# Kernel optimization log

Measured on AMD Instinct MI355X. Metric: run time of the kernel, lower is better.

The kernel has to match this reference:

```python
import jax, jax.numpy as jnp
import numpy as np

T, N, F0, H0, H1 = 8, 50000, 128, 128, 64
NNZ, E = 800000, 1000000


def setup_inputs() -> dict:
    key = jax.random.key(0)
    ks = jax.random.split(key, 24)
    s = 0.05  # param scale so sigmoid/tanh gates are not fully saturated
    inp = {
        "X": jax.random.normal(ks[0], (T, N, F0), jnp.float32),
        "A_rows": jax.random.randint(ks[1], (T, NNZ), 0, N, jnp.int32),
        "A_cols": jax.random.randint(ks[2], (T, NNZ), 0, N, jnp.int32),
        "A_val": jax.random.uniform(ks[3], (T, NNZ), jnp.float32),
        "edge_time": jax.random.randint(ks[4], (E,), 0, T, jnp.int32),
        "edge_src": jax.random.randint(ks[5], (E,), 0, N, jnp.int32),
        "edge_trg": jax.random.randint(ks[6], (E,), 0, N, jnp.int32),
        "p": jax.random.normal(ks[7], (F0,), jnp.float32),
        "W_Z": s * jax.random.normal(ks[8], (F0, F0), jnp.float32),
        "U_Z": s * jax.random.normal(ks[9], (F0, F0), jnp.float32),
        "B_Z": s * jax.random.normal(ks[10], (F0, H0), jnp.float32),
        "W_R": s * jax.random.normal(ks[11], (F0, F0), jnp.float32),
        "U_R": s * jax.random.normal(ks[12], (F0, F0), jnp.float32),
        "B_R": s * jax.random.normal(ks[13], (F0, H0), jnp.float32),
        "W_H": s * jax.random.normal(ks[14], (F0, F0), jnp.float32),
        "U_H": s * jax.random.normal(ks[15], (F0, F0), jnp.float32),
        "B_H": s * jax.random.normal(ks[16], (F0, H0), jnp.float32),
        "W_init": s * jax.random.normal(ks[17], (F0, H0), jnp.float32),
        "U": s * jax.random.normal(ks[18], (2 * H0, H1), jnp.float32),
    }
    return inp


def reference(X, A_rows, A_cols, A_val, edge_time, edge_src, edge_trg,
              p, W_Z, U_Z, B_Z, W_R, U_R, B_R, W_H, U_H, B_H, W_init, U):
    Tn, Nn, _ = X.shape
    k = W_init.shape[1]  # topk size == columns of evolving weight
    p_hat = p / jnp.linalg.norm(p)

    def step(W, inputs):
        Xs, rows, cols, vals = inputs  # Xs: [N,F0]; rows/cols/vals: [NNZ]
        # summarize: top-k node rows weighted by projection score
        y = Xs @ p_hat                       # [N]
        topv, idx = jax.lax.top_k(y, k)
        Z = (Xs[idx] * topv[:, None]).T      # [F0,k]
        # GRU-style weight evolution on the [F0,k] weight matrix
        Zg = jax.nn.sigmoid(W_Z @ Z + U_Z @ W + B_Z)
        R = jax.nn.sigmoid(W_R @ Z + U_R @ W + B_R)
        Ht = jnp.tanh(W_H @ Z + U_H @ (R * W) + B_H)
        W_new = (1.0 - Zg) * W + Zg * Ht
        # sparse GCN conv: (A @ Xs) @ W_new  via gather + segment_sum
        AH = jax.ops.segment_sum(vals[:, None] * Xs[cols], rows,
                                 num_segments=Nn)  # [N,F0]
        return W_new, AH @ W_new                   # Y_t: [N,H0]

    W_fin, Y = jax.lax.scan(step, W_init, (X, A_rows, A_cols, A_val))
    Yf = Y.reshape(Tn * Nn, -1)                    # [T*N,H0]
    flat_src = edge_time * Nn + edge_src
    flat_trg = edge_time * Nn + edge_trg
    Y_mat = jnp.concatenate([Yf[flat_src], Yf[flat_trg]], axis=1)  # [E,2*H0]
    output = Y_mat @ U                              # [E,H1]
    return output, W_fin
```

## Files before the change

### kernel.cpp

```cpp
#include <hip/hip_runtime.h>
#include <math.h>

#define T_ 8
#define N_ 50000
#define F0_ 128
#define H0_ 128
#define H1_ 64
#define NNZ_ 800000
#define E_ 1000000
#define K_ 128
#define CAP_ 3072
#define NB 391
#define BCH 8192

__device__ inline unsigned ford(float f) {
    unsigned b = __float_as_uint(f);
    return (b & 0x80000000u) ? ~b : (b | 0x80000000u);
}
__device__ inline float funord(unsigned u) {
    unsigned b = (u & 0x80000000u) ? (u & 0x7fffffffu) : ~u;
    return __uint_as_float(b);
}
__device__ inline unsigned bfr(float f) {
    unsigned u = __float_as_uint(f);
    return (u + 0x7fffu + ((u >> 16) & 1u)) >> 16;
}
__device__ inline unsigned bfpack(float lo, float hi) { return bfr(lo) | (bfr(hi) << 16); }
__device__ inline float bflo(unsigned u) { return __uint_as_float(u << 16); }
__device__ inline float bfhi(unsigned u) { return __uint_as_float(u & 0xffff0000u); }

__global__ void k_phat(const float* p, float* p_hat) {
    __shared__ float s[128];
    int i = threadIdx.x;
    float v = p[i];
    s[i] = v * v;
    __syncthreads();
    for (int off = 64; off > 0; off >>= 1) {
        if (i < off) s[i] += s[i + off];
        __syncthreads();
    }
    p_hat[i] = v / sqrtf(s[0]);
}

__global__ void k_y(const float* __restrict__ X, const float* __restrict__ p_hat,
                    float* __restrict__ y, unsigned* __restrict__ Xh) {
    int gid = blockIdx.x * 256 + threadIdx.x;
    int wave = gid >> 6, lane = gid & 63;
    if (wave >= T_ * N_) return;
    const float2* xr = (const float2*)(X + (size_t)wave * F0_);
    float2 a = xr[lane];
    if (Xh) Xh[(size_t)wave * 64 + lane] = bfpack(a.x, a.y);
    float2 ph = ((const float2*)p_hat)[lane];
    float acc = a.x * ph.x + a.y * ph.y;
#pragma unroll
    for (int off = 32; off > 0; off >>= 1) acc += __shfl_down(acc, off);
    if (lane == 0) y[wave] = acc;
}

__global__ __launch_bounds__(1024) void k_topk(const float* __restrict__ y,
                                               float* __restrict__ topv,
                                               int* __restrict__ topidx) {
    int t = blockIdx.x;
    const float* yt = y + (size_t)t * N_;
    __shared__ int hist[256];
    __shared__ int sb1, sAbove, sP, scand;
    __shared__ unsigned cu[CAP_];
    __shared__ int cidx[CAP_];
    int tid = threadIdx.x;

    if (tid < 256) hist[tid] = 0;
    __syncthreads();
    for (int i = tid; i < N_; i += 1024) {
        unsigned u = ford(yt[i]);
        atomicAdd(&hist[u >> 24], 1);
    }
    __syncthreads();
    if (tid == 0) {
        int acc = 0, b = 255;
        for (; b >= 0; b--) { acc += hist[b]; if (acc >= K_) break; }
        sb1 = b;
        sAbove = acc - hist[b];
    }
    __syncthreads();
    int b1 = sb1;
    if (tid < 256) hist[tid] = 0;
    __syncthreads();
    for (int i = tid; i < N_; i += 1024) {
        unsigned u = ford(yt[i]);
        if ((int)(u >> 24) == b1) atomicAdd(&hist[(u >> 16) & 255], 1);
    }
    __syncthreads();
    if (tid == 0) {
        int acc = sAbove, b = 255;
        for (; b >= 0; b--) { acc += hist[b]; if (acc >= K_) break; }
        sP = (b1 << 8) | b;
        scand = 0;
    }
    __syncthreads();
    unsigned P = (unsigned)sP;
    for (int i = tid; i < N_; i += 1024) {
        unsigned u = ford(yt[i]);
        if ((u >> 16) >= P) {
            int pos = atomicAdd(&scand, 1);
            if (pos < CAP_) { cu[pos] = u; cidx[pos] = i; }
        }
    }
    __syncthreads();
    int C = min(scand, CAP_);
    for (int c = tid; c < C; c += 1024) {
        unsigned uc = cu[c];
        int ic = cidx[c];
        int rank = 0;
        for (int o = 0; o < C; o++) {
            unsigned uo = cu[o];
            rank += (uo > uc) || (uo == uc && cidx[o] < ic);
        }
        if (rank < K_) {
            topv[t * K_ + rank] = funord(uc);
            topidx[t * K_ + rank] = ic;
        }
    }
}

__global__ void k_z(const float* __restrict__ X, const float* __restrict__ topv,
                    const int* __restrict__ topidx, float* __restrict__ Z) {
    int gid = blockIdx.x * 256 + threadIdx.x;
    if (gid >= T_ * F0_ * K_) return;
    int j = gid & 127;
    int f = (gid >> 7) & 127;
    int t = gid >> 14;
    int idx = topidx[t * K_ + j];
    float v = topv[t * K_ + j];
    Z[gid] = X[((size_t)(t * N_ + idx)) * F0_ + f] * v;
}

__global__ void k_az(const float* __restrict__ WZ, const float* __restrict__ WR,
                     const float* __restrict__ WH, const float* __restrict__ BZ,
                     const float* __restrict__ BR, const float* __restrict__ BH,
                     const float* __restrict__ Z, float* __restrict__ AZ,
                     float* __restrict__ AR, float* __restrict__ AHo) {
    int gid = blockIdx.x * 256 + threadIdx.x;
    int j = gid & 127;
    int i = (gid >> 7) & 127;
    int t = (gid >> 14) & 7;
    int g = gid >> 17;
    const float* W = (g == 0) ? WZ : (g == 1) ? WR : WH;
    const float* B = (g == 0) ? BZ : (g == 1) ? BR : BH;
    float* Ao = (g == 0) ? AZ : (g == 1) ? AR : AHo;
    const float* Zt = Z + (size_t)t * 16384;
    float acc = B[i * 128 + j];
    for (int k = 0; k < 128; k++) acc += W[i * 128 + k] * Zt[k * 128 + j];
    Ao[(size_t)(t * 128 + i) * 128 + j] = acc;
}

__global__ __launch_bounds__(512) void k_cnt(const int* __restrict__ A_rows,
                                             int* __restrict__ bcnt) {
    __shared__ int cnt[NB];
    int t = blockIdx.y, ci = blockIdx.x;
    int tid = threadIdx.x;
    for (int i = tid; i < NB; i += 512) cnt[i] = 0;
    __syncthreads();
    int e0 = ci * BCH;
#pragma unroll
    for (int k = 0; k < 16; k++) {
        int idx = e0 + tid + k * 512;
        if (idx < NNZ_) atomicAdd(&cnt[A_rows[(size_t)t * NNZ_ + idx] >> 7], 1);
    }
    __syncthreads();
    for (int b = tid; b < NB; b += 512)
        if (cnt[b]) atomicAdd(&bcnt[t * NB + b], cnt[b]);
}

__global__ __launch_bounds__(512) void k_bscan(const int* __restrict__ bcnt,
                                               int* __restrict__ bbase) {
    int t = blockIdx.x;
    int tid = threadIdx.x;
    __shared__ int buf[512];
    int v = (tid < NB) ? bcnt[t * NB + tid] : 0;
    buf[tid] = v;
    __syncthreads();
    for (int off = 1; off < 512; off <<= 1) {
        int x = (tid >= off) ? buf[tid - off] : 0;
        __syncthreads();
        buf[tid] += x;
        __syncthreads();
    }
    if (tid < NB) bbase[t * NB + tid] = buf[tid] - v;
}

__global__ __launch_bounds__(512) void k_binA(const int* __restrict__ A_rows,
                                              const int* __restrict__ A_cols,
                                              const float* __restrict__ A_val,
                                              const int* __restrict__ bbase,
                                              int* __restrict__ bfill,
                                              int2* __restrict__ ebuck) {
    __shared__ int cnt[NB];
    __shared__ int gbase[NB];
    __shared__ int rbase[NB];
    int t = blockIdx.y, ci = blockIdx.x;
    int tid = threadIdx.x;
    for (int i = tid; i < NB; i += 512) cnt[i] = 0;
    __syncthreads();
    unsigned meta[16];
    float val[16];
    int lrank[16];
    int e0 = ci * BCH;
#pragma unroll
    for (int k = 0; k < 16; k++) {
        int idx = e0 + tid + k * 512;
        meta[k] = 0xFFFFFFFFu;
        val[k] = 0.f;
        lrank[k] = 0;
        if (idx < NNZ_) {
            int r = A_rows[(size_t)t * NNZ_ + idx];
            int c = A_cols[(size_t)t * NNZ_ + idx];
            val[k] = A_val[(size_t)t * NNZ_ + idx];
            int b = r >> 7, rlo = r & 127;
            meta[k] = (unsigned)c | ((unsigned)rlo << 16) | ((unsigned)b << 23);
            lrank[k] = atomicAdd(&cnt[b], 1);
        }
    }
    __syncthreads();
    for (int b = tid; b < NB; b += 512) {
        int n = cnt[b];
        gbase[b] = n ? atomicAdd(&bfill[t * NB + b], n) : 0;
        rbase[b] = bbase[t * NB + b];
    }
    __syncthreads();
#pragma unroll
    for (int k = 0; k < 16; k++) {
        if (meta[k] != 0xFFFFFFFFu) {
            int b = meta[k] >> 23;
            ebuck[(size_t)t * NNZ_ + rbase[b] + gbase[b] + lrank[k]] =
                make_int2((int)meta[k], __float_as_int(val[k]));
        }
    }
}

__global__ __launch_bounds__(256) void k_bsort(const int* __restrict__ bbase,
                                               const int* __restrict__ bcnt,
                                               const int2* __restrict__ ebuck,
                                               int2* __restrict__ ecv,
                                               int* __restrict__ row_ptr) {
    __shared__ int rcnt[128];
    __shared__ int rex[128];
    __shared__ int rfill[128];
    __shared__ int sbuf[128];
    int t = blockIdx.y, b = blockIdx.x;
    int tid = threadIdx.x;
    int r0 = b << 7;
    int nrows = min(128, N_ - r0);
    int base = bbase[t * NB + b];
    int n = bcnt[t * NB + b];
    if (tid < 128) {
        rcnt[tid] = 0;
        rfill[tid] = 0;
    }
    __syncthreads();
    const int2* src = ebuck + (size_t)t * NNZ_ + base;
    int2* dst = ecv + (size_t)t * NNZ_ + base;
    for (int i = tid; i < n; i += 256) atomicAdd(&rcnt[(src[i].x >> 16) & 127], 1);
    __syncthreads();
    if (tid < 128) sbuf[tid] = rcnt[tid];
    __syncthreads();
    for (int off = 1; off < 128; off <<= 1) {
        int x = (tid >= off && tid < 128) ? sbuf[tid - off] : 0;
        __syncthreads();
        if (tid < 128) sbuf[tid] += x;
        __syncthreads();
    }
    if (tid < 128) rex[tid] = sbuf[tid] - rcnt[tid];
    if (tid < nrows) row_ptr[(size_t)t * (N_ + 1) + r0 + tid] = base + sbuf[tid] - rcnt[tid];
    if (b == 0 && tid == 0) row_ptr[(size_t)t * (N_ + 1) + N_] = NNZ_;
    __syncthreads();
    for (int i = tid; i < n; i += 256) {
        int2 e = src[i];
        int rlo = (e.x >> 16) & 127;
        int col = e.x & 0xFFFF;
        int pos = rex[rlo] + atomicAdd(&rfill[rlo], 1);
        dst[pos] = make_int2(col, e.y);
    }
}

__global__ __launch_bounds__(256) void k_xwu(const unsigned* __restrict__ Xh,
                                             const float* __restrict__ WU,
                                             unsigned* __restrict__ XWU) {
    __shared__ float AT[32][36];
    __shared__ float WUc[32][128];
    int t = blockIdx.y;
    int rbase = blockIdx.x * 32;
    int tid = threadIdx.x;
    const float* wu = WU + (size_t)t * 16384;
    const unsigned* Xt = Xh + (size_t)t * N_ * 64;
    unsigned* XWUt = XWU + (size_t)t * N_ * 64;
    int cg = tid & 31;
    int rg = tid >> 5;
    float4 acc0 = {0.f, 0.f, 0.f, 0.f};
    float4 acc1 = {0.f, 0.f, 0.f, 0.f};
    float4 acc2 = {0.f, 0.f, 0.f, 0.f};
    float4 acc3 = {0.f, 0.f, 0.f, 0.f};
    int srow = tid >> 3;
    int sk4 = (tid & 7) * 4;
    for (int kc = 0; kc < 128; kc += 32) {
        {
            uint2 u = {0u, 0u};
            int r = rbase + srow;
            if (r < N_) u = *(const uint2*)(Xt + (size_t)r * 64 + (kc >> 1) + (sk4 >> 1));
            AT[sk4 + 0][srow] = bflo(u.x);
            AT[sk4 + 1][srow] = bfhi(u.x);
            AT[sk4 + 2][srow] = bflo(u.y);
            AT[sk4 + 3][srow] = bfhi(u.y);
        }
        {
            const float4* src = (const float4*)(wu + (size_t)kc * 128);
            float4* dst = (float4*)&WUc[0][0];
            dst[tid] = src[tid];
            dst[tid + 256] = src[tid + 256];
            dst[tid + 512] = src[tid + 512];
            dst[tid + 768] = src[tid + 768];
        }
        __syncthreads();
#pragma unroll 4
        for (int kk = 0; kk < 32; kk++) {
            float4 a = *(const float4*)&AT[kk][rg * 4];
            float4 w = *(const float4*)&WUc[kk][cg * 4];
            acc0.x += a.x * w.x; acc0.y += a.x * w.y; acc0.z += a.x * w.z; acc0.w += a.x * w.w;
            acc1.x += a.y * w.x; acc1.y += a.y * w.y; acc1.z += a.y * w.z; acc1.w += a.y * w.w;
            acc2.x += a.z * w.x; acc2.y += a.z * w.y; acc2.z += a.z * w.z; acc2.w += a.z * w.w;
            acc3.x += a.w * w.x; acc3.y += a.w * w.y; acc3.z += a.w * w.z; acc3.w += a.w * w.w;
        }
        __syncthreads();
    }
    int r0 = rbase + rg * 4;
    if (r0 + 0 < N_) {
        uint2 o = {bfpack(acc0.x, acc0.y), bfpack(acc0.z, acc0.w)};
        *(uint2*)(XWUt + (size_t)(r0 + 0) * 64 + cg * 2) = o;
    }
    if (r0 + 1 < N_) {
        uint2 o = {bfpack(acc1.x, acc1.y), bfpack(acc1.z, acc1.w)};
        *(uint2*)(XWUt + (size_t)(r0 + 1) * 64 + cg * 2) = o;
    }
    if (r0 + 2 < N_) {
        uint2 o = {bfpack(acc2.x, acc2.y), bfpack(acc2.z, acc2.w)};
        *(uint2*)(XWUt + (size_t)(r0 + 2) * 64 + cg * 2) = o;
    }
    if (r0 + 3 < N_) {
        uint2 o = {bfpack(acc3.x, acc3.y), bfpack(acc3.z, acc3.w)};
        *(uint2*)(XWUt + (size_t)(r0 + 3) * 64 + cg * 2) = o;
    }
}

__global__ void k_spmm2(const unsigned* __restrict__ XWU, const int* __restrict__ row_ptr,
                        const int2* __restrict__ ecv, unsigned* __restrict__ PQh) {
    int gid = blockIdx.x * 256 + threadIdx.x;
    int wave = gid >> 6, lane = gid & 63;
    if (wave >= T_ * N_) return;
    int t = wave / N_;
    int r = wave - t * N_;
    int s = row_ptr[(size_t)t * (N_ + 1) + r];
    int len = row_ptr[(size_t)t * (N_ + 1) + r + 1] - s;
    const unsigned* Xt = XWU + (size_t)t * N_ * 64 + lane;
    const int2* ev = ecv + (size_t)t * NNZ_;
    float2 acc = {0.f, 0.f};
    for (int base = 0; base < len; base += 64) {
        int nn = min(64, len - base);
        int2 my = {0, 0};
        if (base + lane < len) my = ev[s + base + lane];
        int q = 0;
        for (; q + 16 <= nn; q += 16) {
            int c0 = __shfl(my.x, q + 0);  float v0 = __int_as_float(__shfl(my.y, q + 0));
            int c1 = __shfl(my.x, q + 1);  float v1 = __int_as_float(__shfl(my.y, q + 1));
            int c2 = __shfl(my.x, q + 2);  float v2 = __int_as_float(__shfl(my.y, q + 2));
            int c3 = __shfl(my.x, q + 3);  float v3 = __int_as_float(__shfl(my.y, q + 3));
            int c4 = __shfl(my.x, q + 4);  float v4 = __int_as_float(__shfl(my.y, q + 4));
            int c5 = __shfl(my.x, q + 5);  float v5 = __int_as_float(__shfl(my.y, q + 5));
            int c6 = __shfl(my.x, q + 6);  float v6 = __int_as_float(__shfl(my.y, q + 6));
            int c7 = __shfl(my.x, q + 7);  float v7 = __int_as_float(__shfl(my.y, q + 7));
            int c8 = __shfl(my.x, q + 8);  float v8 = __int_as_float(__shfl(my.y, q + 8));
            int c9 = __shfl(my.x, q + 9);  float v9 = __int_as_float(__shfl(my.y, q + 9));
            int cA = __shfl(my.x, q + 10); float vA = __int_as_float(__shfl(my.y, q + 10));
            int cB = __shfl(my.x, q + 11); float vB = __int_as_float(__shfl(my.y, q + 11));
            int cC = __shfl(my.x, q + 12); float vC = __int_as_float(__shfl(my.y, q + 12));
            int cD = __shfl(my.x, q + 13); float vD = __int_as_float(__shfl(my.y, q + 13));
            int cE = __shfl(my.x, q + 14); float vE = __int_as_float(__shfl(my.y, q + 14));
            int cF = __shfl(my.x, q + 15); float vF = __int_as_float(__shfl(my.y, q + 15));
            unsigned x0 = Xt[(size_t)c0 * 64];
            unsigned x1 = Xt[(size_t)c1 * 64];
            unsigned x2 = Xt[(size_t)c2 * 64];
            unsigned x3 = Xt[(size_t)c3 * 64];
            unsigned x4 = Xt[(size_t)c4 * 64];
            unsigned x5 = Xt[(size_t)c5 * 64];
            unsigned x6 = Xt[(size_t)c6 * 64];
            unsigned x7 = Xt[(size_t)c7 * 64];
            unsigned x8 = Xt[(size_t)c8 * 64];
            unsigned x9 = Xt[(size_t)c9 * 64];
            unsigned xA = Xt[(size_t)cA * 64];
            unsigned xB = Xt[(size_t)cB * 64];
            unsigned xC = Xt[(size_t)cC * 64];
            unsigned xD = Xt[(size_t)cD * 64];
            unsigned xE = Xt[(size_t)cE * 64];
            unsigned xF = Xt[(size_t)cF * 64];
            acc.x += v0 * bflo(x0); acc.y += v0 * bfhi(x0);
            acc.x += v1 * bflo(x1); acc.y += v1 * bfhi(x1);
            acc.x += v2 * bflo(x2); acc.y += v2 * bfhi(x2);
            acc.x += v3 * bflo(x3); acc.y += v3 * bfhi(x3);
            acc.x += v4 * bflo(x4); acc.y += v4 * bfhi(x4);
            acc.x += v5 * bflo(x5); acc.y += v5 * bfhi(x5);
            acc.x += v6 * bflo(x6); acc.y += v6 * bfhi(x6);
            acc.x += v7 * bflo(x7); acc.y += v7 * bfhi(x7);
            acc.x += v8 * bflo(x8); acc.y += v8 * bfhi(x8);
            acc.x += v9 * bflo(x9); acc.y += v9 * bfhi(x9);
            acc.x += vA * bflo(xA); acc.y += vA * bfhi(xA);
            acc.x += vB * bflo(xB); acc.y += vB * bfhi(xB);
            acc.x += vC * bflo(xC); acc.y += vC * bfhi(xC);
            acc.x += vD * bflo(xD); acc.y += vD * bfhi(xD);
            acc.x += vE * bflo(xE); acc.y += vE * bfhi(xE);
            acc.x += vF * bflo(xF); acc.y += vF * bfhi(xF);
        }
        for (; q + 8 <= nn; q += 8) {
            int c0 = __shfl(my.x, q + 0); float v0 = __int_as_float(__shfl(my.y, q + 0));
            int c1 = __shfl(my.x, q + 1); float v1 = __int_as_float(__shfl(my.y, q + 1));
            int c2 = __shfl(my.x, q + 2); float v2 = __int_as_float(__shfl(my.y, q + 2));
            int c3 = __shfl(my.x, q + 3); float v3 = __int_as_float(__shfl(my.y, q + 3));
            int c4 = __shfl(my.x, q + 4); float v4 = __int_as_float(__shfl(my.y, q + 4));
            int c5 = __shfl(my.x, q + 5); float v5 = __int_as_float(__shfl(my.y, q + 5));
            int c6 = __shfl(my.x, q + 6); float v6 = __int_as_float(__shfl(my.y, q + 6));
            int c7 = __shfl(my.x, q + 7); float v7 = __int_as_float(__shfl(my.y, q + 7));
            unsigned x0 = Xt[(size_t)c0 * 64];
            unsigned x1 = Xt[(size_t)c1 * 64];
            unsigned x2 = Xt[(size_t)c2 * 64];
            unsigned x3 = Xt[(size_t)c3 * 64];
            unsigned x4 = Xt[(size_t)c4 * 64];
            unsigned x5 = Xt[(size_t)c5 * 64];
            unsigned x6 = Xt[(size_t)c6 * 64];
            unsigned x7 = Xt[(size_t)c7 * 64];
            acc.x += v0 * bflo(x0); acc.y += v0 * bfhi(x0);
            acc.x += v1 * bflo(x1); acc.y += v1 * bfhi(x1);
            acc.x += v2 * bflo(x2); acc.y += v2 * bfhi(x2);
            acc.x += v3 * bflo(x3); acc.y += v3 * bfhi(x3);
            acc.x += v4 * bflo(x4); acc.y += v4 * bfhi(x4);
            acc.x += v5 * bflo(x5); acc.y += v5 * bfhi(x5);
            acc.x += v6 * bflo(x6); acc.y += v6 * bfhi(x6);
            acc.x += v7 * bflo(x7); acc.y += v7 * bfhi(x7);
        }
        for (; q < nn; q++) {
            int c = __shfl(my.x, q);
            float v = __int_as_float(__shfl(my.y, q));
            unsigned xp = Xt[(size_t)c * 64];
            acc.x += v * bflo(xp);
            acc.y += v * bfhi(xp);
        }
    }
    PQh[(size_t)wave * 64 + lane] = bfpack(acc.x, acc.y);
}

__global__ void k_spmm_f32(const float* __restrict__ X, const int* __restrict__ row_ptr,
                           const int2* __restrict__ ecv, float* __restrict__ AH) {
    int gid = blockIdx.x * 256 + threadIdx.x;
    int wave = gid >> 6, lane = gid & 63;
    if (wave >= T_ * N_) return;
    int t = wave / N_;
    int r = wave - t * N_;
    int s = row_ptr[(size_t)t * (N_ + 1) + r];
    int len = row_ptr[(size_t)t * (N_ + 1) + r + 1] - s;
    const float2* Xt = (const float2*)(X + (size_t)t * N_ * F0_);
    const int2* ev = ecv + (size_t)t * NNZ_;
    float2 acc = {0.f, 0.f};
    for (int base = 0; base < len; base += 64) {
        int nn = min(64, len - base);
        int2 my = {0, 0};
        if (base + lane < len) my = ev[s + base + lane];
        for (int q = 0; q < nn; q++) {
            int c = __shfl(my.x, q);
            float v = __int_as_float(__shfl(my.y, q));
            float2 x = Xt[(size_t)c * 64 + lane];
            acc.x += v * x.x;
            acc.y += v * x.y;
        }
    }
    ((float2*)AH)[(size_t)wave * 64 + lane] = acc;
}

__global__ __launch_bounds__(256) void k_gru(const float* __restrict__ AZt,
                                             const float* __restrict__ ARt,
                                             const float* __restrict__ AHt,
                                             const float* __restrict__ UZ,
                                             const float* __restrict__ UR,
                                             const float* __restrict__ UH,
                                             const float* __restrict__ Wprev,
                                             float* __restrict__ Wnew) {
    __shared__ float RWs[128][2];
    int jl = threadIdx.x >> 7;
    int i = threadIdx.x & 127;
    int j = blockIdx.x * 2 + jl;
    int gid = i * 128 + j;
    float az = AZt[gid], ar = ARt[gid];
    for (int k = 0; k < 128; k++) {
        float w = Wprev[k * 128 + j];
        az += UZ[i * 128 + k] * w;
        ar += UR[i * 128 + k] * w;
    }
    float zg = 1.f / (1.f + expf(-az));
    float rg = 1.f / (1.f + expf(-ar));
    RWs[i][jl] = rg * Wprev[gid];
    __syncthreads();
    float acc = AHt[gid];
    for (int k = 0; k < 128; k++) acc += UH[i * 128 + k] * RWs[k][jl];
    float ht = tanhf(acc);
    float w0 = Wprev[gid];
    Wnew[gid] = (1.f - zg) * w0 + zg * ht;
}

__global__ void k_wu(const float* __restrict__ W_seq, const float* __restrict__ U,
                     float* __restrict__ WU) {
    int blk = blockIdx.x;
    int t = blk >> 7, k = blk & 127;
    int h2 = threadIdx.x;
    const float* Wt = W_seq + (size_t)t * 16384;
    int h = h2 & 63;
    const float* Ub = U + (h2 < 64 ? 0 : 128 * 64);
    float acc = 0.f;
    for (int m = 0; m < 128; m++) acc += Wt[k * 128 + m] * Ub[m * 64 + h];
    WU[((size_t)t * 128 + k) * 128 + h2] = acc;
}

__global__ __launch_bounds__(256) void k_pq_f32(float* __restrict__ AH,
                                                const float* __restrict__ WU) {
    __shared__ float AT[32][36];
    __shared__ float WUc[32][128];
    int t = blockIdx.y;
    int rbase = blockIdx.x * 32;
    int tid = threadIdx.x;
    const float* wu = WU + (size_t)t * 16384;
    float* AHt = AH + (size_t)t * N_ * F0_;
    int cg = tid & 31;
    int rg = tid >> 5;
    float4 acc0 = {0.f, 0.f, 0.f, 0.f};
    float4 acc1 = {0.f, 0.f, 0.f, 0.f};
    float4 acc2 = {0.f, 0.f, 0.f, 0.f};
    float4 acc3 = {0.f, 0.f, 0.f, 0.f};
    int srow = tid >> 3;
    int sk4 = (tid & 7) * 4;
    for (int kc = 0; kc < 128; kc += 32) {
        {
            float4 v = {0.f, 0.f, 0.f, 0.f};
            int r = rbase + srow;
            if (r < N_) v = *(const float4*)(AHt + (size_t)r * F0_ + kc + sk4);
            AT[sk4 + 0][srow] = v.x;
            AT[sk4 + 1][srow] = v.y;
            AT[sk4 + 2][srow] = v.z;
            AT[sk4 + 3][srow] = v.w;
        }
        {
            const float4* src = (const float4*)(wu + (size_t)kc * 128);
            float4* dst = (float4*)&WUc[0][0];
            dst[tid] = src[tid];
            dst[tid + 256] = src[tid + 256];
            dst[tid + 512] = src[tid + 512];
            dst[tid + 768] = src[tid + 768];
        }
        __syncthreads();
#pragma unroll 4
        for (int kk = 0; kk < 32; kk++) {
            float4 a = *(const float4*)&AT[kk][rg * 4];
            float4 w = *(const float4*)&WUc[kk][cg * 4];
            acc0.x += a.x * w.x; acc0.y += a.x * w.y; acc0.z += a.x * w.z; acc0.w += a.x * w.w;
            acc1.x += a.y * w.x; acc1.y += a.y * w.y; acc1.z += a.y * w.z; acc1.w += a.y * w.w;
            acc2.x += a.z * w.x; acc2.y += a.z * w.y; acc2.z += a.z * w.z; acc2.w += a.z * w.w;
            acc3.x += a.w * w.x; acc3.y += a.w * w.y; acc3.z += a.w * w.z; acc3.w += a.w * w.w;
        }
        __syncthreads();
    }
    int r0 = rbase + rg * 4;
    if (r0 + 0 < N_) *(float4*)(AHt + (size_t)(r0 + 0) * F0_ + cg * 4) = acc0;
    if (r0 + 1 < N_) *(float4*)(AHt + (size_t)(r0 + 1) * F0_ + cg * 4) = acc1;
    if (r0 + 2 < N_) *(float4*)(AHt + (size_t)(r0 + 2) * F0_ + cg * 4) = acc2;
    if (r0 + 3 < N_) *(float4*)(AHt + (size_t)(r0 + 3) * F0_ + cg * 4) = acc3;
}

__global__ void k_final(const unsigned* __restrict__ PQh, const int* __restrict__ et,
                        const int* __restrict__ es, const int* __restrict__ eg,
                        float* __restrict__ out) {
    int gid = blockIdx.x * 256 + threadIdx.x;
    if (gid >= E_ * 16) return;
    int e = gid >> 4, q = gid & 15;
    int t = et[e];
    const uint2 a = *(const uint2*)(PQh + ((size_t)(t * N_ + es[e])) * 64 + q * 2);
    const uint2 b = *(const uint2*)(PQh + ((size_t)(t * N_ + eg[e])) * 64 + 32 + q * 2);
    float4 o;
    o.x = bflo(a.x) + bflo(b.x);
    o.y = bfhi(a.x) + bfhi(b.x);
    o.z = bflo(a.y) + bflo(b.y);
    o.w = bfhi(a.y) + bfhi(b.y);
    *(float4*)(out + (size_t)e * 64 + q * 4) = o;
}

__global__ void k_final_f32(const float* __restrict__ PQ, const int* __restrict__ et,
                            const int* __restrict__ es, const int* __restrict__ eg,
                            float* __restrict__ out) {
    int gid = blockIdx.x * 256 + threadIdx.x;
    if (gid >= E_ * 16) return;
    int e = gid >> 4, q = gid & 15;
    int t = et[e];
    const float4 a = *(const float4*)(PQ + ((size_t)(t * N_ + es[e])) * 128 + q * 4);
    const float4 b = *(const float4*)(PQ + ((size_t)(t * N_ + eg[e])) * 128 + 64 + q * 4);
    float4 o = {a.x + b.x, a.y + b.y, a.z + b.z, a.w + b.w};
    *(float4*)(out + (size_t)e * 64 + q * 4) = o;
}

__global__ void k_wfin(const float* __restrict__ W_seq, float* __restrict__ out) {
    int gid = blockIdx.x * 256 + threadIdx.x;
    out[(size_t)E_ * 64 + gid] = W_seq[(size_t)7 * 16384 + gid];
}

extern "C" void kernel_launch(void* const* d_in, const int* in_sizes, int n_in,
                              void* d_out, int out_size, void* d_ws, size_t ws_size,
                              hipStream_t stream) {
    const float* X = (const float*)d_in[0];
    const int* A_rows = (const int*)d_in[1];
    const int* A_cols = (const int*)d_in[2];
    const float* A_val = (const float*)d_in[3];
    const int* edge_time = (const int*)d_in[4];
    const int* edge_src = (const int*)d_in[5];
    const int* edge_trg = (const int*)d_in[6];
    const float* p = (const float*)d_in[7];
    const float* W_Z = (const float*)d_in[8];
    const float* U_Z = (const float*)d_in[9];
    const float* B_Z = (const float*)d_in[10];
    const float* W_R = (const float*)d_in[11];
    const float* U_R = (const float*)d_in[12];
    const float* B_R = (const float*)d_in[13];
    const float* W_H = (const float*)d_in[14];
    const float* U_H = (const float*)d_in[15];
    const float* B_H = (const float*)d_in[16];
    const float* W_init = (const float*)d_in[17];
    const float* U = (const float*)d_in[18];
    float* out = (float*)d_out;

    char* ws = (char*)d_ws;
    size_t off = 0;
    auto take = [&](size_t bytes) {
        char* ptr = ws + off;
        off = (off + bytes + 255) & ~(size_t)255;
        return (void*)ptr;
    };
    float* AHreg = (float*)take((size_t)T_ * N_ * F0_ * 4);
    int2* ecv = (int2*)take((size_t)T_ * NNZ_ * 8);
    float* yv = (float*)take((size_t)T_ * N_ * 4);
    int* row_ptr = (int*)take((size_t)T_ * (N_ + 1) * 4);
    int* bcnt = (int*)take((size_t)T_ * NB * 4);
    int* bbase = (int*)take((size_t)T_ * NB * 4);
    int* bfill = (int*)take((size_t)T_ * NB * 4);
    float* p_hat = (float*)take(512);
    float* topv = (float*)take((size_t)T_ * K_ * 4);
    int* topidx = (int*)take((size_t)T_ * K_ * 4);
    float* Z = (float*)take((size_t)T_ * F0_ * K_ * 4);
    float* AZb = (float*)take((size_t)T_ * 16384 * 4);
    float* ARb = (float*)take((size_t)T_ * 16384 * 4);
    float* AHb = (float*)take((size_t)T_ * 16384 * 4);
    float* W_seq = (float*)take((size_t)T_ * 16384 * 4);
    float* WU = (float*)take((size_t)T_ * 16384 * 4);
    unsigned* Xh = (unsigned*)take((size_t)T_ * N_ * 64 * 4);
    bool use_bf16 = (off <= ws_size);
    int2* ebuck = (int2*)AHreg;
    unsigned* XWU = (unsigned*)AHreg;
    unsigned* PQh = XWU + (size_t)T_ * N_ * 64;

    hipMemsetAsync(bcnt, 0, (size_t)T_ * NB * 4, stream);
    hipMemsetAsync(bfill, 0, (size_t)T_ * NB * 4, stream);

    k_phat<<<1, 128, 0, stream>>>(p, p_hat);
    k_y<<<(T_ * N_ * 64) / 256, 256, 0, stream>>>(X, p_hat, yv, use_bf16 ? Xh : nullptr);
    k_topk<<<T_, 1024, 0, stream>>>(yv, topv, topidx);
    k_z<<<(T_ * F0_ * K_) / 256, 256, 0, stream>>>(X, topv, topidx, Z);
    k_az<<<(3 * T_ * 16384) / 256, 256, 0, stream>>>(W_Z, W_R, W_H, B_Z, B_R, B_H, Z,
                                                     AZb, ARb, AHb);
    {
        dim3 gA((NNZ_ + BCH - 1) / BCH, T_);
        k_cnt<<<gA, 512, 0, stream>>>(A_rows, bcnt);
        k_bscan<<<T_, 512, 0, stream>>>(bcnt, bbase);
        k_binA<<<gA, 512, 0, stream>>>(A_rows, A_cols, A_val, bbase, bfill, ebuck);
        dim3 gB(NB, T_);
        k_bsort<<<gB, 256, 0, stream>>>(bbase, bcnt, ebuck, ecv, row_ptr);
    }
    for (int t = 0; t < T_; t++) {
        const float* Wprev = (t == 0) ? W_init : (W_seq + (size_t)(t - 1) * 16384);
        k_gru<<<64, 256, 0, stream>>>(AZb + (size_t)t * 16384, ARb + (size_t)t * 16384,
                                      AHb + (size_t)t * 16384, U_Z, U_R, U_H, Wprev,
                                      W_seq + (size_t)t * 16384);
    }
    k_wu<<<T_ * 128, 128, 0, stream>>>(W_seq, U, WU);
    if (use_bf16) {
        dim3 g((N_ + 31) / 32, T_);
        k_xwu<<<g, 256, 0, stream>>>(Xh, WU, XWU);
        k_spmm2<<<(T_ * N_ * 64) / 256, 256, 0, stream>>>(XWU, row_ptr, ecv, PQh);
        k_final<<<(E_ * 16) / 256, 256, 0, stream>>>(PQh, edge_time, edge_src,
                                                     edge_trg, out);
    } else {
        float* AH = AHreg;
        k_spmm_f32<<<(T_ * N_ * 64) / 256, 256, 0, stream>>>(X, row_ptr, ecv, AH);
        dim3 g((N_ + 31) / 32, T_);
        k_pq_f32<<<g, 256, 0, stream>>>(AH, WU);
        k_final_f32<<<(E_ * 16) / 256, 256, 0, stream>>>(AH, edge_time, edge_src,
                                                         edge_trg, out);
    }
    k_wfin<<<(F0_ * H0_) / 256, 256, 0, stream>>>(W_seq, out);
}
```

Before: 954.4 us.

## Fuse GRU timesteps into one kernel and widen SpMM gathers to half-wave pairs

The eight per-timestep GRU launches become a single kernel. Each block owns two columns of W across all timesteps, which is valid because each column's recurrence depends only on that same column, and it keeps the column in shared memory and writes a transposed W sequence. k_wu and k_wfin are changed to read the transposed layout. Separately, the SpMM kernel now has each half-wave process alternate nonzeros using 8-byte gathers with four accumulators, then combines the two halves with a shuffle. This halves the number of gather instructions per row, in exchange for extra shuffles and select logic.

```diff
diff --git a/kernel.cpp b/kernel.cpp
--- a/kernel.cpp
+++ b/kernel.cpp
@@ -280,6 +280,60 @@
         int pos = rex[rlo] + atomicAdd(&rfill[rlo], 1);
         dst[pos] = make_int2(col, e.y);
     }
+}
+
+__global__ __launch_bounds__(256) void k_gru8(const float* __restrict__ AZb,
+                                              const float* __restrict__ ARb,
+                                              const float* __restrict__ AHb,
+                                              const float* __restrict__ UZ,
+                                              const float* __restrict__ UR,
+                                              const float* __restrict__ UH,
+                                              const float* __restrict__ W_init,
+                                              float* __restrict__ WT) {
+    __shared__ float Wc[128][2];
+    __shared__ float RWs[128][2];
+    int jl = threadIdx.x >> 7;
+    int i = threadIdx.x & 127;
+    int j = blockIdx.x * 2 + jl;
+    Wc[i][jl] = W_init[i * 128 + j];
+    __syncthreads();
+    for (int t = 0; t < T_; t++) {
+        const float* AZt = AZb + (size_t)t * 16384;
+        const float* ARt = ARb + (size_t)t * 16384;
+        const float* AHt = AHb + (size_t)t * 16384;
+        float az = AZt[i * 128 + j], ar = ARt[i * 128 + j];
+        for (int k = 0; k < 128; k++) {
+            float w = Wc[k][jl];
+            az += UZ[i * 128 + k] * w;
+            ar += UR[i * 128 + k] * w;
+        }
+        float zg = 1.f / (1.f + expf(-az));
+        float rg = 1.f / (1.f + expf(-ar));
+        float wself = Wc[i][jl];
+        RWs[i][jl] = rg * wself;
+        __syncthreads();
+        float acc = AHt[i * 128 + j];
+        for (int k = 0; k < 128; k++) acc += UH[i * 128 + k] * RWs[k][jl];
+        float ht = tanhf(acc);
+        float nw = (1.f - zg) * wself + zg * ht;
+        __syncthreads();
+        Wc[i][jl] = nw;
+        WT[((size_t)t * 128 + j) * 128 + i] = nw;
+        __syncthreads();
+    }
+}
+
+__global__ void k_wu(const float* __restrict__ WT, const float* __restrict__ U,
+                     float* __restrict__ WU) {
+    int blk = blockIdx.x;
+    int t = blk >> 7, k = blk & 127;
+    int h2 = threadIdx.x;
+    int h = h2 & 63;
+    const float* Ub = U + (h2 < 64 ? 0 : 128 * 64);
+    float acc = 0.f;
+    for (int m = 0; m < 128; m++)
+        acc += WT[((size_t)t * 128 + m) * 128 + k] * Ub[m * 64 + h];
+    WU[((size_t)t * 128 + k) * 128 + h2] = acc;
 }
 
 __global__ __launch_bounds__(256) void k_xwu(const unsigned* __restrict__ Xh,
@@ -350,6 +404,14 @@
     }
 }
 
+#define PAIRSEL(J, QOFF)                                                        \
+    {                                                                           \
+        int cl = __shfl(my.x, (QOFF) + 2 * J), ch = __shfl(my.x, (QOFF) + 2 * J + 1); \
+        int vl = __shfl(my.y, (QOFF) + 2 * J), vh = __shfl(my.y, (QOFF) + 2 * J + 1); \
+        c##J = hl ? ch : cl;                                                    \
+        v##J = __int_as_float(hl ? vh : vl);                                    \
+    }
+
 __global__ void k_spmm2(const unsigned* __restrict__ XWU, const int* __restrict__ row_ptr,
                         const int2* __restrict__ ecv, unsigned* __restrict__ PQh) {
     int gid = blockIdx.x * 256 + threadIdx.x;
@@ -359,99 +421,60 @@
     int r = wave - t * N_;
     int s = row_ptr[(size_t)t * (N_ + 1) + r];
     int len = row_ptr[(size_t)t * (N_ + 1) + r + 1] - s;
-    const unsigned* Xt = XWU + (size_t)t * N_ * 64 + lane;
+    int hl = lane >> 5;
+    const uint2* Xt2 = (const uint2*)(XWU + (size_t)t * N_ * 64) + (lane & 31);
     const int2* ev = ecv + (size_t)t * NNZ_;
-    float2 acc = {0.f, 0.f};
+    float4 acc = {0.f, 0.f, 0.f, 0.f};
     for (int base = 0; base < len; base += 64) {
         int nn = min(64, len - base);
         int2 my = {0, 0};
         if (base + lane < len) my = ev[s + base + lane];
         int q = 0;
         for (; q + 16 <= nn; q += 16) {
-            int c0 = __shfl(my.x, q + 0);  float v0 = __int_as_float(__shfl(my.y, q + 0));
-            int c1 = __shfl(my.x, q + 1);  float v1 = __int_as_float(__shfl(my.y, q + 1));
-            int c2 = __shfl(my.x, q + 2);  float v2 = __int_as_float(__shfl(my.y, q + 2));
-            int c3 = __shfl(my.x, q + 3);  float v3 = __int_as_float(__shfl(my.y, q + 3));
-            int c4 = __shfl(my.x, q + 4);  float v4 = __int_as_float(__shfl(my.y, q + 4));
-            int c5 = __shfl(my.x, q + 5);  float v5 = __int_as_float(__shfl(my.y, q + 5));
-            int c6 = __shfl(my.x, q + 6);  float v6 = __int_as_float(__shfl(my.y, q + 6));
-            int c7 = __shfl(my.x, q + 7);  float v7 = __int_as_float(__shfl(my.y, q + 7));
-            int c8 = __shfl(my.x, q + 8);  float v8 = __int_as_float(__shfl(my.y, q + 8));
-            int c9 = __shfl(my.x, q + 9);  float v9 = __int_as_float(__shfl(my.y, q + 9));
-            int cA = __shfl(my.x, q + 10); float vA = __int_as_float(__shfl(my.y, q + 10));
-            int cB = __shfl(my.x, q + 11); float vB = __int_as_float(__shfl(my.y, q + 11));
-            int cC = __shfl(my.x, q + 12); float vC = __int_as_float(__shfl(my.y, q + 12));
-            int cD = __shfl(my.x, q + 13); float vD = __int_as_float(__shfl(my.y, q + 13));
-            int cE = __shfl(my.x, q + 14); float vE = __int_as_float(__shfl(my.y, q + 14));
-            int cF = __shfl(my.x, q + 15); float vF = __int_as_float(__shfl(my.y, q + 15));
-            unsigned x0 = Xt[(size_t)c0 * 64];
-            unsigned x1 = Xt[(size_t)c1 * 64];
-            unsigned x2 = Xt[(size_t)c2 * 64];
-            unsigned x3 = Xt[(size_t)c3 * 64];
-            unsigned x4 = Xt[(size_t)c4 * 64];
-            unsigned x5 = Xt[(size_t)c5 * 64];
-            unsigned x6 = Xt[(size_t)c6 * 64];
-            unsigned x7 = Xt[(size_t)c7 * 64];
-            unsigned x8 = Xt[(size_t)c8 * 64];
-            unsigned x9 = Xt[(size_t)c9 * 64];
-            unsigned xA = Xt[(size_t)cA * 64];
-            unsigned xB = Xt[(size_t)cB * 64];
-            unsigned xC = Xt[(size_t)cC * 64];
-            unsigned xD = Xt[(size_t)cD * 64];
-            unsigned xE = Xt[(size_t)cE * 64];
-            unsigned xF = Xt[(size_t)cF * 64];
-            acc.x += v0 * bflo(x0); acc.y += v0 * bfhi(x0);
-            acc.x += v1 * bflo(x1); acc.y += v1 * bfhi(x1);
-            acc.x += v2 * bflo(x2); acc.y += v2 * bfhi(x2);
-            acc.x += v3 * bflo(x3); acc.y += v3 * bfhi(x3);
-            acc.x += v4 * bflo(x4); acc.y += v4 * bfhi(x4);
-            acc.x += v5 * bflo(x5); acc.y += v5 * bfhi(x5);
-            acc.x += v6 * bflo(x6); acc.y += v6 * bfhi(x6);
-            acc.x += v7 * bflo(x7); acc.y += v7 * bfhi(x7);
-            acc.x += v8 * bflo(x8); acc.y += v8 * bfhi(x8);
-            acc.x += v9 * bflo(x9); acc.y += v9 * bfhi(x9);
-            acc.x += vA * bflo(xA); acc.y += vA * bfhi(xA);
-            acc.x += vB * bflo(xB); acc.y += vB * bfhi(xB);
-            acc.x += vC * bflo(xC); acc.y += vC * bfhi(xC);
-            acc.x += vD * bflo(xD); acc.y += vD * bfhi(xD);
-            acc.x += vE * bflo(xE); acc.y += vE * bfhi(xE);
-            acc.x += vF * bflo(xF); acc.y += vF * bfhi(xF);
-        }
-        for (; q + 8 <= nn; q += 8) {
-            int c0 = __shfl(my.x, q + 0); float v0 = __int_as_float(__shfl(my.y, q + 0));
-            int c1 = __shfl(my.x, q + 1); float v1 = __int_as_float(__shfl(my.y, q + 1));
-            int c2 = __shfl(my.x, q + 2); float v2 = __int_as_float(__shfl(my.y, q + 2));
-            int c3 = __shfl(my.x, q + 3); float v3 = __int_as_float(__shfl(my.y, q + 3));
-            int c4 = __shfl(my.x, q + 4); float v4 = __int_as_float(__shfl(my.y, q + 4));
-            int c5 = __shfl(my.x, q + 5); float v5 = __int_as_float(__shfl(my.y, q + 5));
-            int c6 = __shfl(my.x, q + 6); float v6 = __int_as_float(__shfl(my.y, q + 6));
-            int c7 = __shfl(my.x, q + 7); float v7 = __int_as_float(__shfl(my.y, q + 7));
-            unsigned x0 = Xt[(size_t)c0 * 64];
-            unsigned x1 = Xt[(size_t)c1 * 64];
-            unsigned x2 = Xt[(size_t)c2 * 64];
-            unsigned x3 = Xt[(size_t)c3 * 64];
-            unsigned x4 = Xt[(size_t)c4 * 64];
-            unsigned x5 = Xt[(size_t)c5 * 64];
-            unsigned x6 = Xt[(size_t)c6 * 64];
-            unsigned x7 = Xt[(size_t)c7 * 64];
-            acc.x += v0 * bflo(x0); acc.y += v0 * bfhi(x0);
-            acc.x += v1 * bflo(x1); acc.y += v1 * bfhi(x1);
-            acc.x += v2 * bflo(x2); acc.y += v2 * bfhi(x2);
-            acc.x += v3 * bflo(x3); acc.y += v3 * bfhi(x3);
-            acc.x += v4 * bflo(x4); acc.y += v4 * bfhi(x4);
-            acc.x += v5 * bflo(x5); acc.y += v5 * bfhi(x5);
-            acc.x += v6 * bflo(x6); acc.y += v6 * bfhi(x6);
-            acc.x += v7 * bflo(x7); acc.y += v7 * bfhi(x7);
-        }
-        for (; q < nn; q++) {
+            int c0, c1, c2, c3, c4, c5, c6, c7;
+            float v0, v1, v2, v3, v4, v5, v6, v7;
+            PAIRSEL(0, q) PAIRSEL(1, q) PAIRSEL(2, q) PAIRSEL(3, q)
+            PAIRSEL(4, q) PAIRSEL(5, q) PAIRSEL(6, q) PAIRSEL(7, q)
+            uint2 x0 = Xt2[(size_t)c0 * 32];
+            uint2 x1 = Xt2[(size_t)c1 * 32];
+            uint2 x2 = Xt2[(size_t)c2 * 32];
+            uint2 x3 = Xt2[(size_t)c3 * 32];
+            uint2 x4 = Xt2[(size_t)c4 * 32];
+            uint2 x5 = Xt2[(size_t)c5 * 32];
+            uint2 x6 = Xt2[(size_t)c6 * 32];
+            uint2 x7 = Xt2[(size_t)c7 * 32];
+            acc.x += v0 * bflo(x0.x); acc.y += v0 * bfhi(x0.x); acc.z += v0 * bflo(x0.y); acc.w += v0 * bfhi(x0.y);
+            acc.x += v1 * bflo(x1.x); acc.y += v1 * bfhi(x1.x); acc.z += v1 * bflo(x1.y); acc.w += v1 * bfhi(x1.y);
+            acc.x += v2 * bflo(x2.x); acc.y += v2 * bfhi(x2.x); acc.z += v2 * bflo(x2.y); acc.w += v2 * bfhi(x2.y);
+            acc.x += v3 * bflo(x3.x); acc.y += v3 * bfhi(x3.x); acc.z += v3 * bflo(x3.y); acc.w += v3 * bfhi(x3.y);
+            acc.x += v4 * bflo(x4.x); acc.y += v4 * bfhi(x4.x); acc.z += v4 * bflo(x4.y); acc.w += v4 * bfhi(x4.y);
+            acc.x += v5 * bflo(x5.x); acc.y += v5 * bfhi(x5.x); acc.z += v5 * bflo(x5.y); acc.w += v5 * bfhi(x5.y);
+            acc.x += v6 * bflo(x6.x); acc.y += v6 * bfhi(x6.x); acc.z += v6 * bflo(x6.y); acc.w += v6 * bfhi(x6.y);
+            acc.x += v7 * bflo(x7.x); acc.y += v7 * bfhi(x7.x); acc.z += v7 * bflo(x7.y); acc.w += v7 * bfhi(x7.y);
+        }
+        for (; q + 2 <= nn; q += 2) {
+            int c0;
+            float v0;
+            PAIRSEL(0, q)
+            uint2 x0 = Xt2[(size_t)c0 * 32];
+            acc.x += v0 * bflo(x0.x); acc.y += v0 * bfhi(x0.x); acc.z += v0 * bflo(x0.y); acc.w += v0 * bfhi(x0.y);
+        }
+        if (q < nn) {
             int c = __shfl(my.x, q);
             float v = __int_as_float(__shfl(my.y, q));
-            unsigned xp = Xt[(size_t)c * 64];
-            acc.x += v * bflo(xp);
-            acc.y += v * bfhi(xp);
-        }
-    }
-    PQh[(size_t)wave * 64 + lane] = bfpack(acc.x, acc.y);
+            if (hl) v = 0.f;
+            uint2 x = Xt2[(size_t)c * 32];
+            acc.x += v * bflo(x.x); acc.y += v * bfhi(x.x); acc.z += v * bflo(x.y); acc.w += v * bfhi(x.y);
+        }
+    }
+    acc.x += __shfl_down(acc.x, 32);
+    acc.y += __shfl_down(acc.y, 32);
+    acc.z += __shfl_down(acc.z, 32);
+    acc.w += __shfl_down(acc.w, 32);
+    if (lane < 32) {
+        uint2 o = {bfpack(acc.x, acc.y), bfpack(acc.z, acc.w)};
+        *((uint2*)(PQh + (size_t)wave * 64) + lane) = o;
+    }
 }
 
 __global__ void k_spmm_f32(const float* __restrict__ X, const int* __restrict__ row_ptr,
@@ -479,49 +502,6 @@
         }
     }
     ((float2*)AH)[(size_t)wave * 64 + lane] = acc;
-}
-
-__global__ __launch_bounds__(256) void k_gru(const float* __restrict__ AZt,
-                                             const float* __restrict__ ARt,
-                                             const float* __restrict__ AHt,
-                                             const float* __restrict__ UZ,
-                                             const float* __restrict__ UR,
-                                             const float* __restrict__ UH,
-                                             const float* __restrict__ Wprev,
-                                             float* __restrict__ Wnew) {
-    __shared__ float RWs[128][2];
-    int jl = threadIdx.x >> 7;
-    int i = threadIdx.x & 127;
-    int j = blockIdx.x * 2 + jl;
-    int gid = i * 128 + j;
-    float az = AZt[gid], ar = ARt[gid];
-    for (int k = 0; k < 128; k++) {
-        float w = Wprev[k * 128 + j];
-        az += UZ[i * 128 + k] * w;
-        ar += UR[i * 128 + k] * w;
-    }
-    float zg = 1.f / (1.f + expf(-az));
-    float rg = 1.f / (1.f + expf(-ar));
-    RWs[i][jl] = rg * Wprev[gid];
-    __syncthreads();
-    float acc = AHt[gid];
-    for (int k = 0; k < 128; k++) acc += UH[i * 128 + k] * RWs[k][jl];
-    float ht = tanhf(acc);
-    float w0 = Wprev[gid];
-    Wnew[gid] = (1.f - zg) * w0 + zg * ht;
-}
-
-__global__ void k_wu(const float* __restrict__ W_seq, const float* __restrict__ U,
-                     float* __restrict__ WU) {
-    int blk = blockIdx.x;
-    int t = blk >> 7, k = blk & 127;
-    int h2 = threadIdx.x;
-    const float* Wt = W_seq + (size_t)t * 16384;
-    int h = h2 & 63;
-    const float* Ub = U + (h2 < 64 ? 0 : 128 * 64);
-    float acc = 0.f;
-    for (int m = 0; m < 128; m++) acc += Wt[k * 128 + m] * Ub[m * 64 + h];
-    WU[((size_t)t * 128 + k) * 128 + h2] = acc;
 }
 
 __global__ __launch_bounds__(256) void k_pq_f32(float* __restrict__ AH,
@@ -608,9 +588,10 @@
     *(float4*)(out + (size_t)e * 64 + q * 4) = o;
 }
 
-__global__ void k_wfin(const float* __restrict__ W_seq, float* __restrict__ out) {
-    int gid = blockIdx.x * 256 + threadIdx.x;
-    out[(size_t)E_ * 64 + gid] = W_seq[(size_t)7 * 16384 + gid];
+__global__ void k_wfin(const float* __restrict__ WT, float* __restrict__ out) {
+    int gid = blockIdx.x * 256 + threadIdx.x;
+    int k = gid >> 7, m = gid & 127;
+    out[(size_t)E_ * 64 + gid] = WT[(size_t)7 * 16384 + m * 128 + k];
 }
 
 extern "C" void kernel_launch(void* const* d_in, const int* in_sizes, int n_in,
@@ -658,7 +639,7 @@
     float* AZb = (float*)take((size_t)T_ * 16384 * 4);
     float* ARb = (float*)take((size_t)T_ * 16384 * 4);
     float* AHb = (float*)take((size_t)T_ * 16384 * 4);
-    float* W_seq = (float*)take((size_t)T_ * 16384 * 4);
+    float* WT = (float*)take((size_t)T_ * 16384 * 4);
     float* WU = (float*)take((size_t)T_ * 16384 * 4);
     unsigned* Xh = (unsigned*)take((size_t)T_ * N_ * 64 * 4);
     bool use_bf16 = (off <= ws_size);
@@ -683,13 +664,8 @@
         dim3 gB(NB, T_);
         k_bsort<<<gB, 256, 0, stream>>>(bbase, bcnt, ebuck, ecv, row_ptr);
     }
-    for (int t = 0; t < T_; t++) {
-        const float* Wprev = (t == 0) ? W_init : (W_seq + (size_t)(t - 1) * 16384);
-        k_gru<<<64, 256, 0, stream>>>(AZb + (size_t)t * 16384, ARb + (size_t)t * 16384,
-                                      AHb + (size_t)t * 16384, U_Z, U_R, U_H, Wprev,
-                                      W_seq + (size_t)t * 16384);
-    }
-    k_wu<<<T_ * 128, 128, 0, stream>>>(W_seq, U, WU);
+    k_gru8<<<64, 256, 0, stream>>>(AZb, ARb, AHb, U_Z, U_R, U_H, W_init, WT);
+    k_wu<<<T_ * 128, 128, 0, stream>>>(WT, U, WU);
     if (use_bf16) {
         dim3 g((N_ + 31) / 32, T_);
         k_xwu<<<g, 256, 0, stream>>>(Xh, WU, XWU);
@@ -704,5 +680,5 @@
         k_final_f32<<<(E_ * 16) / 256, 256, 0, stream>>>(AH, edge_time, edge_src,
                                                          edge_trg, out);
     }
-    k_wfin<<<(F0_ * H0_) / 256, 256, 0, stream>>>(W_seq, out);
-}
+    k_wfin<<<(F0_ * H0_) / 256, 256, 0, stream>>>(WT, out);
+}
```

Result: no change. 937.2 us (-1.8%).

## Fuse eight GRU timesteps into one persistent kernel and use nontemporal output stores

Applied to the files above, without the earlier changes.

Each column of the evolving weight depends only on the same column at the previous step. The eight per-timestep GRU launches are therefore replaced by a single kernel in which every block keeps its two columns in shared memory across all timesteps. The weights are written transposed, and k_wu and k_wfin are adjusted to index that layout. The final edge-output kernels also switch to nontemporal vector stores, so the large streaming output does not pollute cache. This removes seven launches and their global round-trips, at the cost of running the serial recurrence on only 64 blocks.

```diff
diff --git a/kernel.cpp b/kernel.cpp
--- a/kernel.cpp
+++ b/kernel.cpp
@@ -12,6 +12,8 @@
 #define CAP_ 3072
 #define NB 391
 #define BCH 8192
+
+typedef float nf4 __attribute__((ext_vector_type(4)));
 
 __device__ inline unsigned ford(float f) {
     unsigned b = __float_as_uint(f);
@@ -280,6 +282,60 @@
         int pos = rex[rlo] + atomicAdd(&rfill[rlo], 1);
         dst[pos] = make_int2(col, e.y);
     }
+}
+
+__global__ __launch_bounds__(256) void k_gru8(const float* __restrict__ AZb,
+                                              const float* __restrict__ ARb,
+                                              const float* __restrict__ AHb,
+                                              const float* __restrict__ UZ,
+                                              const float* __restrict__ UR,
+                                              const float* __restrict__ UH,
+                                              const float* __restrict__ W_init,
+                                              float* __restrict__ WT) {
+    __shared__ float Wc[128][2];
+    __shared__ float RWs[128][2];
+    int jl = threadIdx.x >> 7;
+    int i = threadIdx.x & 127;
+    int j = blockIdx.x * 2 + jl;
+    Wc[i][jl] = W_init[i * 128 + j];
+    __syncthreads();
+    for (int t = 0; t < T_; t++) {
+        const float* AZt = AZb + (size_t)t * 16384;
+        const float* ARt = ARb + (size_t)t * 16384;
+        const float* AHt = AHb + (size_t)t * 16384;
+        float az = AZt[i * 128 + j], ar = ARt[i * 128 + j];
+        for (int k = 0; k < 128; k++) {
+            float w = Wc[k][jl];
+            az += UZ[i * 128 + k] * w;
+            ar += UR[i * 128 + k] * w;
+        }
+        float zg = 1.f / (1.f + expf(-az));
+        float rg = 1.f / (1.f + expf(-ar));
+        float wself = Wc[i][jl];
+        RWs[i][jl] = rg * wself;
+        __syncthreads();
+        float acc = AHt[i * 128 + j];
+        for (int k = 0; k < 128; k++) acc += UH[i * 128 + k] * RWs[k][jl];
+        float ht = tanhf(acc);
+        float nw = (1.f - zg) * wself + zg * ht;
+        __syncthreads();
+        Wc[i][jl] = nw;
+        WT[((size_t)t * 128 + j) * 128 + i] = nw;
+        __syncthreads();
+    }
+}
+
+__global__ void k_wu(const float* __restrict__ WT, const float* __restrict__ U,
+                     float* __restrict__ WU) {
+    int blk = blockIdx.x;
+    int t = blk >> 7, k = blk & 127;
+    int h2 = threadIdx.x;
+    int h = h2 & 63;
+    const float* Ub = U + (h2 < 64 ? 0 : 128 * 64);
+    float acc = 0.f;
+    for (int m = 0; m < 128; m++)
+        acc += WT[((size_t)t * 128 + m) * 128 + k] * Ub[m * 64 + h];
+    WU[((size_t)t * 128 + k) * 128 + h2] = acc;
 }
 
 __global__ __launch_bounds__(256) void k_xwu(const unsigned* __restrict__ Xh,
@@ -481,49 +537,6 @@
     ((float2*)AH)[(size_t)wave * 64 + lane] = acc;
 }
 
-__global__ __launch_bounds__(256) void k_gru(const float* __restrict__ AZt,
-                                             const float* __restrict__ ARt,
-                                             const float* __restrict__ AHt,
-                                             const float* __restrict__ UZ,
-                                             const float* __restrict__ UR,
-                                             const float* __restrict__ UH,
-                                             const float* __restrict__ Wprev,
-                                             float* __restrict__ Wnew) {
-    __shared__ float RWs[128][2];
-    int jl = threadIdx.x >> 7;
-    int i = threadIdx.x & 127;
-    int j = blockIdx.x * 2 + jl;
-    int gid = i * 128 + j;
-    float az = AZt[gid], ar = ARt[gid];
-    for (int k = 0; k < 128; k++) {
-        float w = Wprev[k * 128 + j];
-        az += UZ[i * 128 + k] * w;
-        ar += UR[i * 128 + k] * w;
-    }
-    float zg = 1.f / (1.f + expf(-az));
-    float rg = 1.f / (1.f + expf(-ar));
-    RWs[i][jl] = rg * Wprev[gid];
-    __syncthreads();
-    float acc = AHt[gid];
-    for (int k = 0; k < 128; k++) acc += UH[i * 128 + k] * RWs[k][jl];
-    float ht = tanhf(acc);
-    float w0 = Wprev[gid];
-    Wnew[gid] = (1.f - zg) * w0 + zg * ht;
-}
-
-__global__ void k_wu(const float* __restrict__ W_seq, const float* __restrict__ U,
-                     float* __restrict__ WU) {
-    int blk = blockIdx.x;
-    int t = blk >> 7, k = blk & 127;
-    int h2 = threadIdx.x;
-    const float* Wt = W_seq + (size_t)t * 16384;
-    int h = h2 & 63;
-    const float* Ub = U + (h2 < 64 ? 0 : 128 * 64);
-    float acc = 0.f;
-    for (int m = 0; m < 128; m++) acc += Wt[k * 128 + m] * Ub[m * 64 + h];
-    WU[((size_t)t * 128 + k) * 128 + h2] = acc;
-}
-
 __global__ __launch_bounds__(256) void k_pq_f32(float* __restrict__ AH,
                                                 const float* __restrict__ WU) {
     __shared__ float AT[32][36];
@@ -587,12 +600,12 @@
     int t = et[e];
     const uint2 a = *(const uint2*)(PQh + ((size_t)(t * N_ + es[e])) * 64 + q * 2);
     const uint2 b = *(const uint2*)(PQh + ((size_t)(t * N_ + eg[e])) * 64 + 32 + q * 2);
-    float4 o;
+    nf4 o;
     o.x = bflo(a.x) + bflo(b.x);
     o.y = bfhi(a.x) + bfhi(b.x);
     o.z = bflo(a.y) + bflo(b.y);
     o.w = bfhi(a.y) + bfhi(b.y);
-    *(float4*)(out + (size_t)e * 64 + q * 4) = o;
+    __builtin_nontemporal_store(o, (nf4*)(out + (size_t)e * 64 + q * 4));
 }
 
 __global__ void k_final_f32(const float* __restrict__ PQ, const int* __restrict__ et,
@@ -604,13 +617,14 @@
     int t = et[e];
     const float4 a = *(const float4*)(PQ + ((size_t)(t * N_ + es[e])) * 128 + q * 4);
     const float4 b = *(const float4*)(PQ + ((size_t)(t * N_ + eg[e])) * 128 + 64 + q * 4);
-    float4 o = {a.x + b.x, a.y + b.y, a.z + b.z, a.w + b.w};
-    *(float4*)(out + (size_t)e * 64 + q * 4) = o;
-}
-
-__global__ void k_wfin(const float* __restrict__ W_seq, float* __restrict__ out) {
+    nf4 o = {a.x + b.x, a.y + b.y, a.z + b.z, a.w + b.w};
+    __builtin_nontemporal_store(o, (nf4*)(out + (size_t)e * 64 + q * 4));
+}
+
+__global__ void k_wfin(const float* __restrict__ WT, float* __restrict__ out) {
     int gid = blockIdx.x * 256 + threadIdx.x;
-    out[(size_t)E_ * 64 + gid] = W_seq[(size_t)7 * 16384 + gid];
+    int k = gid >> 7, m = gid & 127;
+    out[(size_t)E_ * 64 + gid] = WT[(size_t)7 * 16384 + m * 128 + k];
 }
 
 extern "C" void kernel_launch(void* const* d_in, const int* in_sizes, int n_in,
@@ -658,7 +672,7 @@
     float* AZb = (float*)take((size_t)T_ * 16384 * 4);
     float* ARb = (float*)take((size_t)T_ * 16384 * 4);
     float* AHb = (float*)take((size_t)T_ * 16384 * 4);
-    float* W_seq = (float*)take((size_t)T_ * 16384 * 4);
+    float* WT = (float*)take((size_t)T_ * 16384 * 4);
     float* WU = (float*)take((size_t)T_ * 16384 * 4);
     unsigned* Xh = (unsigned*)take((size_t)T_ * N_ * 64 * 4);
     bool use_bf16 = (off <= ws_size);
@@ -683,13 +697,8 @@
         dim3 gB(NB, T_);
         k_bsort<<<gB, 256, 0, stream>>>(bbase, bcnt, ebuck, ecv, row_ptr);
     }
-    for (int t = 0; t < T_; t++) {
-        const float* Wprev = (t == 0) ? W_init : (W_seq + (size_t)(t - 1) * 16384);
-        k_gru<<<64, 256, 0, stream>>>(AZb + (size_t)t * 16384, ARb + (size_t)t * 16384,
-                                      AHb + (size_t)t * 16384, U_Z, U_R, U_H, Wprev,
-                                      W_seq + (size_t)t * 16384);
-    }
-    k_wu<<<T_ * 128, 128, 0, stream>>>(W_seq, U, WU);
+    k_gru8<<<64, 256, 0, stream>>>(AZb, ARb, AHb, U_Z, U_R, U_H, W_init, WT);
+    k_wu<<<T_ * 128, 128, 0, stream>>>(WT, U, WU);
     if (use_bf16) {
         dim3 g((N_ + 31) / 32, T_);
         k_xwu<<<g, 256, 0, stream>>>(Xh, WU, XWU);
@@ -704,5 +713,5 @@
         k_final_f32<<<(E_ * 16) / 256, 256, 0, stream>>>(AH, edge_time, edge_src,
                                                          edge_trg, out);
     }
-    k_wfin<<<(F0_ * H0_) / 256, 256, 0, stream>>>(W_seq, out);
-}
+    k_wfin<<<(F0_ * H0_) / 256, 256, 0, stream>>>(WT, out);
+}
```

After: 910.8 us. 1.05x faster.
